# Kernel tuning notes

Hardware: AMD Instinct MI355X
Metric: run time of the kernel (lower is better)

## Reference

```python
import jax, jax.numpy as jnp
import numpy as np

NUM_HEADS = 8
DIM = 256
HEAD_DIM = DIM // NUM_HEADS  # 32
CPB_HIDDEN = 512
FFN_HIDDEN = 1024


def _relative_position_cpb(query_size, key_size, pretrain_size):
    # TransNeXt-style continuous position bias table + index (query==key grid here)
    qh, qw = query_size
    kh, kw = key_size
    ph, pw = pretrain_size
    aqh = np.arange(qh, dtype=np.float64)
    akh = np.arange(kh, dtype=np.float64)
    aqw = np.arange(qw, dtype=np.float64)
    akw = np.arange(kw, dtype=np.float64)
    kH, kW = np.meshgrid(akh, akw, indexing='ij')
    qH, qW = np.meshgrid(aqh, aqw, indexing='ij')
    rel_h = (qH.reshape(-1)[:, None] - kH.reshape(-1)[None, :]) / (ph - 1) * 8.0
    rel_w = (qW.reshape(-1)[:, None] - kW.reshape(-1)[None, :]) / (pw - 1) * 8.0
    rel = np.stack([rel_h, rel_w], axis=-1).reshape(-1, 2)
    table, idx = np.unique(rel, return_inverse=True, axis=0)
    table = np.sign(table) * np.log2(np.abs(table) + 1.0) / np.log2(8.0)
    return idx.astype(np.int32).reshape(-1), table.astype(np.float32)


def setup_inputs() -> dict:
    key = jax.random.key(0)
    ks = jax.random.split(key, 16)
    B, C, H, W = 8, 256, 128, 128
    q = jax.random.normal(ks[0], (B, C, H, W), dtype=jnp.float32)
    kv = jax.random.normal(ks[1], (B, C, H, W), dtype=jnp.float32)
    rel_idx_np, rel_table_np = _relative_position_cpb((32, 32), (32, 32), (32, 32))
    s = 0.02
    inp = {
        'q': q,
        'kv': kv,
        'rel_pos_index': jnp.asarray(rel_idx_np),
        'rel_coords_table': jnp.asarray(rel_table_np),
        'Wq': jax.random.normal(ks[2], (DIM, DIM), jnp.float32) * s,
        'bq': jnp.zeros((DIM,), jnp.float32),
        'Wkv': jax.random.normal(ks[3], (DIM, 2 * DIM), jnp.float32) * s,
        'bkv': jnp.zeros((2 * DIM,), jnp.float32),
        'Wo': jax.random.normal(ks[4], (DIM, DIM), jnp.float32) * s,
        'bo': jnp.zeros((DIM,), jnp.float32),
        'cpb_w1': jax.random.normal(ks[5], (2, CPB_HIDDEN), jnp.float32) * s,
        'cpb_b1': jnp.zeros((CPB_HIDDEN,), jnp.float32),
        'cpb_w2': jax.random.normal(ks[6], (CPB_HIDDEN, NUM_HEADS), jnp.float32) * s,
        'cpb_b2': jnp.zeros((NUM_HEADS,), jnp.float32),
        'ffn_w1': jax.random.normal(ks[7], (DIM, FFN_HIDDEN), jnp.float32) * s,
        'ffn_b1': jnp.zeros((FFN_HIDDEN,), jnp.float32),
        'ffn_w2': jax.random.normal(ks[8], (FFN_HIDDEN, DIM), jnp.float32) * s,
        'ffn_b2': jnp.zeros((DIM,), jnp.float32),
        'ln_g': jnp.ones((DIM,), jnp.float32),
        'ln_b': jnp.zeros((DIM,), jnp.float32),
    }
    return inp


def _resize_bilinear(x, size):
    # matches torch F.interpolate(mode='bilinear', align_corners=False)
    return jax.image.resize(x, (x.shape[0], x.shape[1], size[0], size[1]),
                            method='linear', antialias=False)


def _layernorm(x, g, b, eps=1e-5):
    mu = jnp.mean(x, axis=-1, keepdims=True)
    var = jnp.mean(jnp.square(x - mu), axis=-1, keepdims=True)
    return (x - mu) * jax.lax.rsqrt(var + eps) * g + b


def _fpn_forward(q, kv, rel_pos_index, rel_coords_table, Wq, bq, Wkv, bkv, Wo, bo,
                 cpb_w1, cpb_b1, cpb_w2, cpb_b2, ffn_w1, ffn_b1, ffn_w2, ffn_b2, ln_g, ln_b):
    x = q
    B, C, H, W = q.shape
    pH = H // 4
    pW = H // 4  # note: original code uses h for both, matching square inputs
    N = pH * pW

    qd = jax.nn.relu(_resize_bilinear(q, (pH, pW)))   # [B,C,pH,pW] (dropout p=0)
    kvd = jax.nn.relu(_resize_bilinear(kv, (pH, pW)))
    qt = qd.reshape(B, C, N).transpose(0, 2, 1)   # [B,N,C]
    kvt = kvd.reshape(B, C, N).transpose(0, 2, 1)  # [B,N,C]

    # --- BVAM: cross-attention with continuous relative position bias ---
    qh = (qt @ Wq + bq).reshape(B, N, NUM_HEADS, HEAD_DIM).transpose(0, 2, 1, 3)  # [B,h,N,d]
    kvp = (kvt @ Wkv + bkv).reshape(B, N, 2, NUM_HEADS, HEAD_DIM).transpose(2, 0, 3, 1, 4)
    k, v = kvp[0], kvp[1]  # [B,h,N,d]

    cpb = jax.nn.relu(rel_coords_table @ cpb_w1 + cpb_b1) @ cpb_w2 + cpb_b2  # [L,h]
    bias = cpb[rel_pos_index].reshape(N, N, NUM_HEADS).transpose(2, 0, 1)    # [h,N,N]

    scale = 1.0 / jnp.sqrt(jnp.float32(HEAD_DIM))
    logits = jnp.einsum('bhnd,bhmd->bhnm', qh, k) * scale + bias[None]
    attn = jax.nn.softmax(logits, axis=-1)
    out = jnp.einsum('bhnm,bhmd->bhnd', attn, v)
    out = out.transpose(0, 2, 1, 3).reshape(B, N, C) @ Wo + bo  # [B,N,C]

    # --- FFN (post-norm, gelu) ---
    ff = jax.nn.gelu(out @ ffn_w1 + ffn_b1, approximate=False) @ ffn_w2 + ffn_b2
    y = _layernorm(out + ff, ln_g, ln_b)  # [B,N,C]

    # back to spatial, upsample, residual
    y = y.transpose(0, 2, 1).reshape(B, C, pH, pW)
    y = jax.nn.relu(_resize_bilinear(y, (H, W)))
    return x + y


def reference(q, kv, rel_pos_index, rel_coords_table, Wq, bq, Wkv, bkv, Wo, bo,
              cpb_w1, cpb_b1, cpb_w2, cpb_b2, ffn_w1, ffn_b1, ffn_w2, ffn_b2, ln_g, ln_b):
    return _fpn_forward(q, kv, rel_pos_index, rel_coords_table, Wq, bq, Wkv, bkv, Wo, bo,
                        cpb_w1, cpb_b1, cpb_w2, cpb_b2, ffn_w1, ffn_b1, ffn_w2, ffn_b2, ln_g, ln_b)
```

## Files before the change

kernel.cpp:

```cpp
#include <hip/hip_runtime.h>
#include <hip/hip_bf16.h>
#include <hip/hip_fp16.h>

typedef __hip_bfloat16 bf16;
typedef __attribute__((ext_vector_type(8))) __bf16 bf16x8;
typedef __attribute__((ext_vector_type(4))) __bf16 bf16x4;
typedef __attribute__((ext_vector_type(4))) float f32x4;
typedef __attribute__((ext_vector_type(4))) float f4;

__device__ __forceinline__ void gload_lds16(const bf16* g, bf16* l)
{
    __builtin_amdgcn_global_load_lds((const __attribute__((address_space(1))) void*)g,
                                     (__attribute__((address_space(3))) void*)l, 16, 0, 0);
}

__global__ __launch_bounds__(256) void prep_kernel(
    const float* __restrict__ tab, const float* __restrict__ w1, const float* __restrict__ b1,
    const float* __restrict__ w2, const float* __restrict__ b2, float* __restrict__ cpbout, int L, int ncpb,
    const float* __restrict__ Wq, const float* __restrict__ Wkv, const float* __restrict__ Wo,
    const float* __restrict__ fw1, const float* __restrict__ fw2,
    bf16* __restrict__ WqT, bf16* __restrict__ WkvT, bf16* __restrict__ WoT,
    bf16* __restrict__ W1T, bf16* __restrict__ W2T,
    const float* __restrict__ qsrc, const float* __restrict__ kvsrc,
    bf16* __restrict__ qdst, bf16* __restrict__ kvdst)
{
    __shared__ float o[32][33];
    const int t = threadIdx.x;
    int bid = blockIdx.x;
    if (bid < ncpb) {
        int l = bid * 32 + (t >> 3);
        int js = t & 7;
        bool valid = l < L;
        float t0 = valid ? tab[2 * l] : 0.f, t1 = valid ? tab[2 * l + 1] : 0.f;
        float acc[8];
#pragma unroll
        for (int hh = 0; hh < 8; ++hh) acc[hh] = 0.f;
        for (int j = js; j < 512; j += 8) {
            float hv = fmaxf(t0 * w1[j] + t1 * w1[512 + j] + b1[j], 0.f);
            f4 w2a = *(const f4*)&w2[j * 8];
            f4 w2b = *(const f4*)&w2[j * 8 + 4];
#pragma unroll
            for (int hh = 0; hh < 4; ++hh) { acc[hh] += hv * w2a[hh]; acc[4 + hh] += hv * w2b[hh]; }
        }
#pragma unroll
        for (int d = 1; d < 8; d <<= 1)
#pragma unroll
            for (int hh = 0; hh < 8; ++hh) acc[hh] += __shfl_xor(acc[hh], d);
        if (js == 0 && valid)
#pragma unroll
            for (int hh = 0; hh < 8; ++hh) cpbout[(size_t)hh * L + l] = acc[hh] + b2[hh];
        return;
    }
    bid -= ncpb;
    if (bid < 3072) {
        const float* W; bf16* WT; int K, N, base;
        if (bid < 256)       { W = Wq;  WT = WqT;  K = 256;  N = 256;  base = 0; }
        else if (bid < 768)  { W = Wkv; WT = WkvT; K = 256;  N = 512;  base = 256; }
        else if (bid < 1024) { W = Wo;  WT = WoT;  K = 256;  N = 256;  base = 768; }
        else if (bid < 2048) { W = fw1; WT = W1T;  K = 256;  N = 1024; base = 1024; }
        else                 { W = fw2; WT = W2T;  K = 1024; N = 256;  base = 2048; }
        int idx = (bid - base) * 256 + t;
        int n = idx / K, k = idx % K;
        WT[idx] = (bf16)W[(size_t)k * N + n];
        return;
    }
    bid -= 3072;
    {
        const float* src = bid < 2048 ? qsrc : kvsrc;
        bf16* dst = bid < 2048 ? qdst : kvdst;
        int bb2 = bid & 2047;
        int cc = bb2 & 7, i = (bb2 >> 3) & 31, b = bb2 >> 8;
#pragma unroll
        for (int p = 0; p < 4; ++p) {
            int id = p * 256 + t;
            int c = id >> 5, j = id & 31;
            const float* r = src + ((size_t)(b * 256 + cc * 32 + c) * 128 + 4 * i + 1) * 128 + 4 * j;
            float4 r1 = *(const float4*)r;
            float4 r2 = *(const float4*)(r + 128);
            o[c][j] = 0.25f * (r1.y + r1.z + r2.y + r2.z);
        }
        __syncthreads();
#pragma unroll
        for (int p = 0; p < 4; ++p) {
            int id = p * 256 + t;
            int j = id >> 5, c = id & 31;
            dst[(size_t)(b * 1024 + i * 32 + j) * 256 + cc * 32 + c] = (bf16)fmaxf(o[c][j], 0.f);
        }
    }
}

__global__ __launch_bounds__(256) void bias_gather_kernel(
    const int* __restrict__ ridx, const float* __restrict__ cpbh,
    bf16* __restrict__ biasF, int L)
{
    __shared__ int rix[32][32];
    const int qt = blockIdx.x, mt = blockIdx.y;
    const int t = threadIdx.x;
    {
        int q = t >> 3, m4 = (t & 7) * 4;
        *(int4*)&rix[q][m4] = *(const int4*)&ridx[(size_t)(qt * 32 + q) * 1024 + mt * 32 + m4];
    }
    __syncthreads();
    const int ls = t & 63, qj = (t >> 6) & 1, hg = t >> 7;
    const int lo = ls & 15, hi = ls >> 4;
    int lidx[8];
#pragma unroll
    for (int j = 0; j < 8; ++j) {
        int kf = j >> 2, r = j & 3;
        lidx[j] = rix[qj * 16 + lo][kf * 16 + hi * 4 + r];
    }
#pragma unroll
    for (int hh = 0; hh < 4; ++hh) {
        int h = hg * 4 + hh;
        const float* ct = cpbh + (size_t)h * L;
        bf16 vals[8];
#pragma unroll
        for (int j = 0; j < 8; ++j) vals[j] = (bf16)ct[lidx[j]];
        size_t off = ((((size_t)(h * 32 + qt) * 32 + mt) * 2 + qj) * 64 + ls) * 8;
        *(bf16x8*)&biasF[off] = *(const bf16x8*)vals;
    }
}

template<int BM, int BN>
__device__ __forceinline__ void gemm_core(
    const bf16* __restrict__ A, const bf16* __restrict__ BT, int K,
    int m0, int n0, bf16* As0, bf16* Bs0, f32x4 (&acc)[BM / 32][BN / 32])
{
    constexpr int MI = BM / 32, NJ = BN / 32;
    const int tid = threadIdx.x;
    const int lane = tid & 63, wid = tid >> 6;
    const int lo = lane & 15, hi = lane >> 4;
    const int wr = wid >> 1, wc = wid & 1;
#pragma unroll
    for (int i = 0; i < MI; ++i)
#pragma unroll
        for (int j = 0; j < NJ; ++j) acc[i][j] = f32x4{0.f, 0.f, 0.f, 0.f};

    auto stage = [&](int bsel, int k0) {
        bf16* As = As0 + bsel * (BM * 64);
        bf16* Bs = Bs0 + bsel * (BN * 64);
#pragma unroll
        for (int p = 0; p < BM / 32; ++p) {
            int f = p * 256 + wid * 64 + lane;
            int row = f >> 3, cs = f & 7;
            gload_lds16(&A[(size_t)(m0 + row) * K + k0 + ((cs ^ (row & 7)) * 8)],
                        As + (size_t)(p * 256 + wid * 64) * 8);
        }
#pragma unroll
        for (int p = 0; p < BN / 32; ++p) {
            int f = p * 256 + wid * 64 + lane;
            int row = f >> 3, cs = f & 7;
            gload_lds16(&BT[(size_t)(n0 + row) * K + k0 + ((cs ^ (row & 7)) * 8)],
                        Bs + (size_t)(p * 256 + wid * 64) * 8);
        }
    };
    stage(0, 0);
    __syncthreads();
    const int nt = K / 64;
    int cur = 0;
    for (int t = 0; t < nt; ++t) {
        if (t + 1 < nt) stage(cur ^ 1, (t + 1) * 64);
        const bf16* As = As0 + cur * (BM * 64);
        const bf16* Bs = Bs0 + cur * (BN * 64);
        bf16x8 af[2][MI], bfr[2][NJ];
#pragma unroll
        for (int kk = 0; kk < 2; ++kk) {
#pragma unroll
            for (int i = 0; i < MI; ++i) {
                int row = wr * (BM / 2) + i * 16 + lo;
                af[kk][i] = *(const bf16x8*)&As[row * 64 + (((kk * 4 + hi) ^ (lo & 7)) * 8)];
            }
#pragma unroll
            for (int j = 0; j < NJ; ++j) {
                int row = wc * (BN / 2) + j * 16 + lo;
                bfr[kk][j] = *(const bf16x8*)&Bs[row * 64 + (((kk * 4 + hi) ^ (lo & 7)) * 8)];
            }
        }
#pragma unroll
        for (int kk = 0; kk < 2; ++kk)
#pragma unroll
            for (int i = 0; i < MI; ++i)
#pragma unroll
                for (int j = 0; j < NJ; ++j)
                    acc[i][j] = __builtin_amdgcn_mfma_f32_16x16x32_bf16(af[kk][i], bfr[kk][j], acc[i][j], 0, 0, 0);
        __syncthreads();
        cur ^= 1;
    }
}

template<int BM, int BN>
__global__ __launch_bounds__(256) void gemm_bt(
    const bf16* __restrict__ A, const bf16* __restrict__ BT,
    const float* __restrict__ bias, bf16* __restrict__ Cb, float* __restrict__ Cf,
    const bf16* __restrict__ resid, int M, int N, int K, int act)
{
    constexpr int MI = BM / 32, NJ = BN / 32;
    __shared__ __align__(16) bf16 As[2 * BM * 64];
    __shared__ __align__(16) bf16 Bs[2 * BN * 64];
    const int tid = threadIdx.x;
    const int lane = tid & 63, wid = tid >> 6;
    const int lo = lane & 15, hi = lane >> 4;
    const int m0 = blockIdx.x * BM, n0 = blockIdx.y * BN;
    const int wr = wid >> 1, wc = wid & 1;
    f32x4 acc[MI][NJ];
    gemm_core<BM, BN>(A, BT, K, m0, n0, As, Bs, acc);
#pragma unroll
    for (int i = 0; i < MI; ++i)
#pragma unroll
        for (int j = 0; j < NJ; ++j) {
            int col = n0 + wc * (BN / 2) + j * 16 + lo;
            float bv = bias[col];
#pragma unroll
            for (int r = 0; r < 4; ++r) {
                int row = m0 + wr * (BM / 2) + i * 16 + hi * 4 + r;
                float v = acc[i][j][r] + bv;
                if (act == 1) v = 0.5f * v * (1.f + erff(v * 0.70710678118654752f));
                if (resid) v += (float)resid[(size_t)row * N + col];
                if (Cb) Cb[(size_t)row * N + col] = (bf16)v;
                else    Cf[(size_t)row * N + col] = v;
            }
        }
}

__global__ __launch_bounds__(256) void gemm_qkv(
    const bf16* __restrict__ qt, const bf16* __restrict__ WqT, const float* __restrict__ bq,
    bf16* __restrict__ qhb,
    const bf16* __restrict__ kvt, const bf16* __restrict__ WkvT, const float* __restrict__ bkv,
    bf16* __restrict__ kvpb)
{
    __shared__ __align__(16) bf16 As[2 * 64 * 64];
    __shared__ __align__(16) bf16 Bs[2 * 64 * 64];
    const int tid = threadIdx.x;
    const int lane = tid & 63, wid = tid >> 6;
    const int lo = lane & 15, hi = lane >> 4;
    const int wr = wid >> 1, wc = wid & 1;
    const int by = blockIdx.y;
    const bf16 *A, *BT; const float* bias; bf16* C; int N, n0;
    if (by < 4) { A = qt;  BT = WqT;  bias = bq;  C = qhb;  N = 256; n0 = by * 64; }
    else        { A = kvt; BT = WkvT; bias = bkv; C = kvpb; N = 512; n0 = (by - 4) * 64; }
    const int m0 = blockIdx.x * 64;
    f32x4 acc[2][2];
    gemm_core<64, 64>(A, BT, 256, m0, n0, As, Bs, acc);
#pragma unroll
    for (int i = 0; i < 2; ++i)
#pragma unroll
        for (int j = 0; j < 2; ++j) {
            int col = n0 + wc * 32 + j * 16 + lo;
            float bv = bias[col];
#pragma unroll
            for (int r = 0; r < 4; ++r) {
                int row = m0 + wr * 32 + i * 16 + hi * 4 + r;
                C[(size_t)row * N + col] = (bf16)(acc[i][j][r] + bv);
            }
        }
}

__global__ __launch_bounds__(256) void ffn2_ln_kernel(
    const bf16* __restrict__ A, const bf16* __restrict__ BT,
    const float* __restrict__ bias, const bf16* __restrict__ resid,
    const float* __restrict__ g, const float* __restrict__ bb,
    bf16* __restrict__ ysp)
{
    __shared__ __align__(16) bf16 As[2 * 32 * 64];
    __shared__ __align__(16) bf16 Bs[2 * 256 * 64];
    __shared__ float buf[32][260];
    const int tid = threadIdx.x;
    const int lane = tid & 63, wid = tid >> 6;
    const int lo = lane & 15, hi = lane >> 4;
    const int m0 = blockIdx.x * 32;
    f32x4 acc[2][4];
#pragma unroll
    for (int i = 0; i < 2; ++i)
#pragma unroll
        for (int j = 0; j < 4; ++j) acc[i][j] = f32x4{0.f, 0.f, 0.f, 0.f};

    auto stage = [&](int bsel, int k0) {
        bf16* Asb = As + bsel * (32 * 64);
        bf16* Bsb = Bs + bsel * (256 * 64);
        {
            int f = tid, row = f >> 3, cs = f & 7;
            gload_lds16(&A[(size_t)(m0 + row) * 1024 + k0 + ((cs ^ (row & 7)) * 8)],
                        Asb + (size_t)(wid * 64) * 8);
        }
#pragma unroll
        for (int p = 0; p < 8; ++p) {
            int f = p * 256 + tid, row = f >> 3, cs = f & 7;
            gload_lds16(&BT[(size_t)row * 1024 + k0 + ((cs ^ (row & 7)) * 8)],
                        Bsb + (size_t)(p * 256 + wid * 64) * 8);
        }
    };
    stage(0, 0);
    __syncthreads();
    int cur = 0;
    for (int t = 0; t < 16; ++t) {
        if (t < 15) stage(cur ^ 1, (t + 1) * 64);
        const bf16* Asb = As + cur * (32 * 64);
        const bf16* Bsb = Bs + cur * (256 * 64);
        bf16x8 af[2][2], bfr[2][4];
#pragma unroll
        for (int kk = 0; kk < 2; ++kk) {
#pragma unroll
            for (int i = 0; i < 2; ++i) {
                int row = i * 16 + lo;
                af[kk][i] = *(const bf16x8*)&Asb[row * 64 + (((kk * 4 + hi) ^ (lo & 7)) * 8)];
            }
#pragma unroll
            for (int j = 0; j < 4; ++j) {
                int row = wid * 64 + j * 16 + lo;
                bfr[kk][j] = *(const bf16x8*)&Bsb[row * 64 + (((kk * 4 + hi) ^ (lo & 7)) * 8)];
            }
        }
#pragma unroll
        for (int kk = 0; kk < 2; ++kk)
#pragma unroll
            for (int i = 0; i < 2; ++i)
#pragma unroll
                for (int j = 0; j < 4; ++j)
                    acc[i][j] = __builtin_amdgcn_mfma_f32_16x16x32_bf16(af[kk][i], bfr[kk][j], acc[i][j], 0, 0, 0);
        __syncthreads();
        cur ^= 1;
    }
#pragma unroll
    for (int i = 0; i < 2; ++i)
#pragma unroll
        for (int j = 0; j < 4; ++j) {
            int col = wid * 64 + j * 16 + lo;
            float bv = bias[col];
#pragma unroll
            for (int r = 0; r < 4; ++r) {
                int lr = i * 16 + hi * 4 + r;
                buf[lr][col] = acc[i][j][r] + bv + (float)resid[(size_t)(m0 + lr) * 256 + col];
            }
        }
    __syncthreads();
#pragma unroll
    for (int rr = 0; rr < 8; ++rr) {
        int row = wid * 8 + rr;
        f4 x = *(const f4*)&buf[row][lane * 4];
        float s = x[0] + x[1] + x[2] + x[3];
#pragma unroll
        for (int d = 1; d < 64; d <<= 1) s += __shfl_xor(s, d);
        float mean = s * (1.f / 256.f);
        f4 dv = {x[0] - mean, x[1] - mean, x[2] - mean, x[3] - mean};
        float s2 = dv[0] * dv[0] + dv[1] * dv[1] + dv[2] * dv[2] + dv[3] * dv[3];
#pragma unroll
        for (int d = 1; d < 64; d <<= 1) s2 += __shfl_xor(s2, d);
        float rstd = rsqrtf(s2 * (1.f / 256.f) + 1e-5f);
        f4 o = {dv[0] * rstd, dv[1] * rstd, dv[2] * rstd, dv[3] * rstd};
        *(f4*)&buf[row][lane * 4] = o;
    }
    __syncthreads();
    float gc = g[tid], bc = bb[tid];
    int b = m0 >> 10, n0l = m0 & 1023;
    bf16* dst = &ysp[((size_t)(b * 256 + tid) << 10) + n0l];
#pragma unroll
    for (int p = 0; p < 4; ++p) {
        bf16 tmp[8];
#pragma unroll
        for (int k = 0; k < 8; ++k) tmp[k] = (bf16)(buf[p * 8 + k][tid] * gc + bc);
        *(bf16x8*)&dst[p * 8] = *(const bf16x8*)tmp;
    }
}

__global__ __launch_bounds__(256) void vtrans_kernel(const bf16* __restrict__ kvp,
                                                     bf16* __restrict__ vT)
{
    __shared__ __align__(16) bf16 tile[64][40];
    int bid = blockIdx.x;
    int mc = bid & 15, h = (bid >> 4) & 7, b = bid >> 7;
    int t = threadIdx.x;
    {
        int m = t >> 2, p = (t & 3) * 8;
        *(float4*)&tile[m][p] =
            *(const float4*)&kvp[(size_t)(b * 1024 + mc * 64 + m) * 512 + 256 + h * 32 + p];
    }
    __syncthreads();
#pragma unroll
    for (int it = 0; it < 8; ++it) {
        int f = it * 256 + t;
        int d = f >> 6, m = f & 63;
        vT[(size_t)((b * 8 + h) * 32 + d) * 1024 + mc * 64 + m] = tile[m][d];
    }
}

__global__ __launch_bounds__(256) void attn_kernel(
    const bf16* __restrict__ qh, const bf16* __restrict__ kvp, const bf16* __restrict__ vT,
    const bf16* __restrict__ biasF, bf16* __restrict__ attnout)
{
    __shared__ __align__(16) bf16 Ps[4][32 * 40];
    __shared__ __align__(16) __half accs[4][32][34];
    __shared__ float pm[4][32], pl[4][32];
    const int tid = threadIdx.x, lane = tid & 63, wid = tid >> 6;
    const int lo = lane & 15, hi = lane >> 4;
    const int qt = blockIdx.x, n0 = qt * 32;
    const int h = blockIdx.y;
    const int b = blockIdx.z;
    const float scale = 0.17677669529663687f;
    const f32x4 zero4 = {0.f, 0.f, 0.f, 0.f};

    bf16x8 qf[2];
#pragma unroll
    for (int qj = 0; qj < 2; ++qj)
        qf[qj] = *(const bf16x8*)&qh[(size_t)(b * 1024 + n0 + qj * 16 + lo) * 256 + h * 32 + hi * 8];

    f32x4 acc[2][2];
#pragma unroll
    for (int i = 0; i < 2; ++i)
#pragma unroll
        for (int j = 0; j < 2; ++j) acc[i][j] = zero4;
    float mrow[2] = {-1e30f, -1e30f}, lrow[2] = {0.f, 0.f};

    bf16* Pw = Ps[wid];

    for (int t = wid; t < 32; t += 4) {
        const int m0 = t * 32;
        bf16x8 kfr0 = *(const bf16x8*)&kvp[(size_t)(b * 1024 + m0 + lo) * 512 + h * 32 + hi * 8];
        bf16x8 kfr1 = *(const bf16x8*)&kvp[(size_t)(b * 1024 + m0 + 16 + lo) * 512 + h * 32 + hi * 8];
        bf16x8 va0 = *(const bf16x8*)&vT[(size_t)((b * 8 + h) * 32 + lo) * 1024 + m0 + hi * 8];
        bf16x8 va1 = *(const bf16x8*)&vT[(size_t)((b * 8 + h) * 32 + 16 + lo) * 1024 + m0 + hi * 8];
        size_t boff = (((size_t)(h * 32 + qt) * 32 + t) * 2 * 64 + lane) * 8;
        bf16x8 bv0 = *(const bf16x8*)&biasF[boff];
        bf16x8 bv1 = *(const bf16x8*)&biasF[boff + 512];

        f32x4 s[2][2];
        s[0][0] = __builtin_amdgcn_mfma_f32_16x16x32_bf16(kfr0, qf[0], zero4, 0, 0, 0);
        s[0][1] = __builtin_amdgcn_mfma_f32_16x16x32_bf16(kfr0, qf[1], zero4, 0, 0, 0);
        s[1][0] = __builtin_amdgcn_mfma_f32_16x16x32_bf16(kfr1, qf[0], zero4, 0, 0, 0);
        s[1][1] = __builtin_amdgcn_mfma_f32_16x16x32_bf16(kfr1, qf[1], zero4, 0, 0, 0);
#pragma unroll
        for (int kf = 0; kf < 2; ++kf)
#pragma unroll
            for (int r = 0; r < 4; ++r) {
                s[kf][0][r] = s[kf][0][r] * scale + (float)bv0[kf * 4 + r];
                s[kf][1][r] = s[kf][1][r] * scale + (float)bv1[kf * 4 + r];
            }
#pragma unroll
        for (int qj = 0; qj < 2; ++qj) {
            float mx = fmaxf(fmaxf(fmaxf(s[0][qj][0], s[0][qj][1]), fmaxf(s[0][qj][2], s[0][qj][3])),
                             fmaxf(fmaxf(s[1][qj][0], s[1][qj][1]), fmaxf(s[1][qj][2], s[1][qj][3])));
            mx = fmaxf(mx, __shfl_xor(mx, 16));
            mx = fmaxf(mx, __shfl_xor(mx, 32));
            float mnew = fmaxf(mrow[qj], mx);
            float alpha = __expf(mrow[qj] - mnew);
            float rs = 0.f;
#pragma unroll
            for (int kf = 0; kf < 2; ++kf)
#pragma unroll
                for (int r = 0; r < 4; ++r) {
                    float p = __expf(s[kf][qj][r] - mnew);
                    s[kf][qj][r] = p;
                    rs += p;
                }
            rs += __shfl_xor(rs, 16);
            rs += __shfl_xor(rs, 32);
            lrow[qj] = lrow[qj] * alpha + rs;
            mrow[qj] = mnew;
#pragma unroll
            for (int di = 0; di < 2; ++di)
#pragma unroll
                for (int r = 0; r < 4; ++r) acc[di][qj][r] *= alpha;
        }
#pragma unroll
        for (int qj = 0; qj < 2; ++qj)
#pragma unroll
            for (int kf = 0; kf < 2; ++kf)
#pragma unroll
                for (int r = 0; r < 4; ++r)
                    Pw[(qj * 16 + lo) * 40 + kf * 16 + hi * 4 + r] = (bf16)s[kf][qj][r];
        bf16x8 pb0 = *(const bf16x8*)&Pw[lo * 40 + hi * 8];
        bf16x8 pb1 = *(const bf16x8*)&Pw[(16 + lo) * 40 + hi * 8];
        acc[0][0] = __builtin_amdgcn_mfma_f32_16x16x32_bf16(va0, pb0, acc[0][0], 0, 0, 0);
        acc[0][1] = __builtin_amdgcn_mfma_f32_16x16x32_bf16(va0, pb1, acc[0][1], 0, 0, 0);
        acc[1][0] = __builtin_amdgcn_mfma_f32_16x16x32_bf16(va1, pb0, acc[1][0], 0, 0, 0);
        acc[1][1] = __builtin_amdgcn_mfma_f32_16x16x32_bf16(va1, pb1, acc[1][1], 0, 0, 0);
    }
#pragma unroll
    for (int di = 0; di < 2; ++di)
#pragma unroll
        for (int qj = 0; qj < 2; ++qj)
#pragma unroll
            for (int r = 0; r < 4; ++r)
                accs[wid][di * 16 + hi * 4 + r][qj * 16 + lo] = __float2half(acc[di][qj][r]);
    if (hi == 0) {
#pragma unroll
        for (int qj = 0; qj < 2; ++qj) {
            pm[wid][qj * 16 + lo] = mrow[qj];
            pl[wid][qj * 16 + lo] = lrow[qj];
        }
    }
    __syncthreads();
    int q = tid >> 3, d0 = (tid & 7) * 4;
    float M = fmaxf(fmaxf(pm[0][q], pm[1][q]), fmaxf(pm[2][q], pm[3][q]));
    float f0 = __expf(pm[0][q] - M), f1 = __expf(pm[1][q] - M);
    float f2 = __expf(pm[2][q] - M), f3 = __expf(pm[3][q] - M);
    float inv = 1.f / (pl[0][q] * f0 + pl[1][q] * f1 + pl[2][q] * f2 + pl[3][q] * f3);
    bf16 tmp[4];
#pragma unroll
    for (int j = 0; j < 4; ++j) {
        int d = d0 + j;
        float o = f0 * (float)accs[0][d][q] + f1 * (float)accs[1][d][q] +
                  f2 * (float)accs[2][d][q] + f3 * (float)accs[3][d][q];
        tmp[j] = (bf16)(o * inv);
    }
    *(bf16x4*)&attnout[(size_t)(b * 1024 + n0 + q) * 256 + h * 32 + d0] = *(const bf16x4*)tmp;
}

__global__ __launch_bounds__(256) void upsample_kernel(const float* __restrict__ x,
    const bf16* __restrict__ ysp, float* __restrict__ out)
{
    int idx = blockIdx.x * 256 + threadIdx.x;
    int w4 = idx & 31; int r1 = idx >> 5;
    int hh = r1 & 127; int r2 = r1 >> 7;
    int c = r2 & 255; int b = r2 >> 8;
    float chh = 0.25f * hh - 0.375f;
    float fi = floorf(chh);
    float fh = chh - fi;
    int i0 = (int)fi;
    int ia = i0 < 0 ? 0 : i0;
    int ib = (i0 + 1) > 31 ? 31 : (i0 + 1);
    const bf16* yr = ysp + ((size_t)(b * 256 + c) << 10);
    const bf16* ra = yr + ia * 32;
    const bf16* rb = yr + ib * 32;
    f4 xv = *(const f4*)&x[(size_t)idx * 4];
    f4 o;
#pragma unroll
    for (int k = 0; k < 4; ++k) {
        int ww = w4 * 4 + k;
        float cww = 0.25f * ww - 0.375f;
        float fj = floorf(cww);
        float fw = cww - fj;
        int j0 = (int)fj;
        int ja = j0 < 0 ? 0 : j0;
        int jb = (j0 + 1) > 31 ? 31 : (j0 + 1);
        float v = (1.f - fh) * ((1.f - fw) * (float)ra[ja] + fw * (float)ra[jb]) +
                  fh * ((1.f - fw) * (float)rb[ja] + fw * (float)rb[jb]);
        o[k] = xv[k] + fmaxf(v, 0.f);
    }
    *(f4*)&out[(size_t)idx * 4] = o;
}

extern "C" void kernel_launch(void* const* d_in, const int* in_sizes, int n_in,
                              void* d_out, int out_size, void* d_ws, size_t ws_size,
                              hipStream_t stream)
{
    (void)n_in; (void)out_size; (void)ws_size;
    const float* q    = (const float*)d_in[0];
    const float* kv   = (const float*)d_in[1];
    const int*   ridx = (const int*)d_in[2];
    const float* rtab = (const float*)d_in[3];
    const float* Wq   = (const float*)d_in[4];
    const float* bq   = (const float*)d_in[5];
    const float* Wkv  = (const float*)d_in[6];
    const float* bkv  = (const float*)d_in[7];
    const float* Wo   = (const float*)d_in[8];
    const float* bo   = (const float*)d_in[9];
    const float* cw1  = (const float*)d_in[10];
    const float* cb1  = (const float*)d_in[11];
    const float* cw2  = (const float*)d_in[12];
    const float* cb2  = (const float*)d_in[13];
    const float* fw1  = (const float*)d_in[14];
    const float* fb1  = (const float*)d_in[15];
    const float* fw2  = (const float*)d_in[16];
    const float* fb2  = (const float*)d_in[17];
    const float* lng  = (const float*)d_in[18];
    const float* lnb  = (const float*)d_in[19];
    const int L = in_sizes[3] / 2;
    const int ncpb = (L + 31) / 32;

    char* w = (char*)d_ws;
    auto alloc = [&](size_t bytes) { char* p = w; w += (bytes + 255) & ~(size_t)255; return p; };
    bf16* qt      = (bf16*)alloc(8192ull * 256 * 2);
    bf16* kvt     = (bf16*)alloc(8192ull * 256 * 2);
    bf16* qhb     = (bf16*)alloc(8192ull * 256 * 2);
    bf16* kvpb    = (bf16*)alloc(8192ull * 512 * 2);
    bf16* vTb     = (bf16*)alloc(8ull * 8 * 32 * 1024 * 2);
    bf16* attnb   = (bf16*)alloc(8192ull * 256 * 2);
    bf16* outb    = (bf16*)alloc(8192ull * 256 * 2);
    bf16* ffh     = (bf16*)alloc(8192ull * 1024 * 2);
    bf16* ysp     = (bf16*)alloc(8ull * 256 * 1024 * 2);
    bf16* WqT     = (bf16*)alloc(256ull * 256 * 2);
    bf16* WkvT    = (bf16*)alloc(512ull * 256 * 2);
    bf16* WoT     = (bf16*)alloc(256ull * 256 * 2);
    bf16* W1T     = (bf16*)alloc(1024ull * 256 * 2);
    bf16* W2T     = (bf16*)alloc(256ull * 1024 * 2);
    float* cpbb   = (float*)alloc((size_t)8 * L * 4);
    bf16* biasF   = ffh;

    prep_kernel<<<dim3(ncpb + 3072 + 4096), 256, 0, stream>>>(
        rtab, cw1, cb1, cw2, cb2, cpbb, L, ncpb,
        Wq, Wkv, Wo, fw1, fw2, WqT, WkvT, WoT, W1T, W2T,
        q, kv, qt, kvt);
    bias_gather_kernel<<<dim3(32, 32), 256, 0, stream>>>(ridx, cpbb, biasF, L);
    gemm_qkv<<<dim3(128, 12), 256, 0, stream>>>(qt, WqT, bq, qhb, kvt, WkvT, bkv, kvpb);
    vtrans_kernel<<<dim3(1024), 256, 0, stream>>>(kvpb, vTb);
    attn_kernel<<<dim3(32, 8, 8), 256, 0, stream>>>(qhb, kvpb, vTb, biasF, attnb);
    gemm_bt<64, 64><<<dim3(128, 4), 256, 0, stream>>>(attnb, WoT, bo, outb, nullptr, nullptr, 8192, 256, 256, 0);
    gemm_bt<128, 64><<<dim3(64, 16), 256, 0, stream>>>(outb, W1T, fb1, ffh, nullptr, nullptr, 8192, 1024, 256, 1);
    ffn2_ln_kernel<<<dim3(256), 256, 0, stream>>>(ffh, W2T, fb2, outb, lng, lnb, ysp);
    upsample_kernel<<<dim3(32768), 256, 0, stream>>>(q, ysp, (float*)d_out);
}
```

Measured before the change: 202.2 us.

## Fuse V transpose into QKV GEMM epilogue and single-buffer GEMM LDS

```diff
diff --git a/kernel.cpp b/kernel.cpp
--- a/kernel.cpp
+++ b/kernel.cpp
@@ -124,7 +124,7 @@
 template<int BM, int BN>
 __device__ __forceinline__ void gemm_core(
     const bf16* __restrict__ A, const bf16* __restrict__ BT, int K,
-    int m0, int n0, bf16* As0, bf16* Bs0, f32x4 (&acc)[BM / 32][BN / 32])
+    int m0, int n0, bf16* As, bf16* Bs, f32x4 (&acc)[BM / 32][BN / 32])
 {
     constexpr int MI = BM / 32, NJ = BN / 32;
     const int tid = threadIdx.x;
@@ -136,9 +136,8 @@
 #pragma unroll
         for (int j = 0; j < NJ; ++j) acc[i][j] = f32x4{0.f, 0.f, 0.f, 0.f};
 
-    auto stage = [&](int bsel, int k0) {
-        bf16* As = As0 + bsel * (BM * 64);
-        bf16* Bs = Bs0 + bsel * (BN * 64);
+    for (int k0 = 0; k0 < K; k0 += 64) {
+        __syncthreads();
 #pragma unroll
         for (int p = 0; p < BM / 32; ++p) {
             int f = p * 256 + wid * 64 + lane;
@@ -153,15 +152,7 @@
             gload_lds16(&BT[(size_t)(n0 + row) * K + k0 + ((cs ^ (row & 7)) * 8)],
                         Bs + (size_t)(p * 256 + wid * 64) * 8);
         }
-    };
-    stage(0, 0);
-    __syncthreads();
-    const int nt = K / 64;
-    int cur = 0;
-    for (int t = 0; t < nt; ++t) {
-        if (t + 1 < nt) stage(cur ^ 1, (t + 1) * 64);
-        const bf16* As = As0 + cur * (BM * 64);
-        const bf16* Bs = Bs0 + cur * (BN * 64);
+        __syncthreads();
         bf16x8 af[2][MI], bfr[2][NJ];
 #pragma unroll
         for (int kk = 0; kk < 2; ++kk) {
@@ -183,8 +174,6 @@
 #pragma unroll
                 for (int j = 0; j < NJ; ++j)
                     acc[i][j] = __builtin_amdgcn_mfma_f32_16x16x32_bf16(af[kk][i], bfr[kk][j], acc[i][j], 0, 0, 0);
-        __syncthreads();
-        cur ^= 1;
     }
 }
 
@@ -195,8 +184,8 @@
     const bf16* __restrict__ resid, int M, int N, int K, int act)
 {
     constexpr int MI = BM / 32, NJ = BN / 32;
-    __shared__ __align__(16) bf16 As[2 * BM * 64];
-    __shared__ __align__(16) bf16 Bs[2 * BN * 64];
+    __shared__ __align__(16) bf16 As[BM * 64];
+    __shared__ __align__(16) bf16 Bs[BN * 64];
     const int tid = threadIdx.x;
     const int lane = tid & 63, wid = tid >> 6;
     const int lo = lane & 15, hi = lane >> 4;
@@ -226,18 +215,18 @@
     const bf16* __restrict__ qt, const bf16* __restrict__ WqT, const float* __restrict__ bq,
     bf16* __restrict__ qhb,
     const bf16* __restrict__ kvt, const bf16* __restrict__ WkvT, const float* __restrict__ bkv,
-    bf16* __restrict__ kvpb)
-{
-    __shared__ __align__(16) bf16 As[2 * 64 * 64];
-    __shared__ __align__(16) bf16 Bs[2 * 64 * 64];
+    bf16* __restrict__ kvpb, bf16* __restrict__ vT)
+{
+    __shared__ __align__(16) bf16 As[64 * 64];
+    __shared__ __align__(16) bf16 Bs[64 * 64];
     const int tid = threadIdx.x;
     const int lane = tid & 63, wid = tid >> 6;
     const int lo = lane & 15, hi = lane >> 4;
     const int wr = wid >> 1, wc = wid & 1;
     const int by = blockIdx.y;
-    const bf16 *A, *BT; const float* bias; bf16* C; int N, n0;
-    if (by < 4) { A = qt;  BT = WqT;  bias = bq;  C = qhb;  N = 256; n0 = by * 64; }
-    else        { A = kvt; BT = WkvT; bias = bkv; C = kvpb; N = 512; n0 = (by - 4) * 64; }
+    const bf16 *A, *BT; const float* bias; int n0;
+    if (by < 4)      { A = qt;  BT = WqT;  bias = bq;  n0 = by * 64; }
+    else             { A = kvt; BT = WkvT; bias = bkv; n0 = (by - 4) * 64; }
     const int m0 = blockIdx.x * 64;
     f32x4 acc[2][2];
     gemm_core<64, 64>(A, BT, 256, m0, n0, As, Bs, acc);
@@ -247,10 +236,27 @@
         for (int j = 0; j < 2; ++j) {
             int col = n0 + wc * 32 + j * 16 + lo;
             float bv = bias[col];
-#pragma unroll
-            for (int r = 0; r < 4; ++r) {
-                int row = m0 + wr * 32 + i * 16 + hi * 4 + r;
-                C[(size_t)row * N + col] = (bf16)(acc[i][j][r] + bv);
+            if (by < 4) {
+#pragma unroll
+                for (int r = 0; r < 4; ++r) {
+                    int row = m0 + wr * 32 + i * 16 + hi * 4 + r;
+                    qhb[(size_t)row * 256 + col] = (bf16)(acc[i][j][r] + bv);
+                }
+            } else if (by < 8) {
+#pragma unroll
+                for (int r = 0; r < 4; ++r) {
+                    int row = m0 + wr * 32 + i * 16 + hi * 4 + r;
+                    kvpb[(size_t)row * 512 + col] = (bf16)(acc[i][j][r] + bv);
+                }
+            } else {
+                int vcol = col - 256;
+                int h = vcol >> 5, d = vcol & 31;
+                int b = m0 >> 10;
+                int mbase = (m0 & 1023) + wr * 32 + i * 16 + hi * 4;
+                bf16 tmp[4];
+#pragma unroll
+                for (int r = 0; r < 4; ++r) tmp[r] = (bf16)(acc[i][j][r] + bv);
+                *(bf16x4*)&vT[(size_t)((b * 8 + h) * 32 + d) * 1024 + mbase] = *(const bf16x4*)tmp;
             }
         }
 }
@@ -261,8 +267,8 @@
     const float* __restrict__ g, const float* __restrict__ bb,
     bf16* __restrict__ ysp)
 {
-    __shared__ __align__(16) bf16 As[2 * 32 * 64];
-    __shared__ __align__(16) bf16 Bs[2 * 256 * 64];
+    __shared__ __align__(16) bf16 As[32 * 64];
+    __shared__ __align__(16) bf16 Bs[256 * 64];
     __shared__ float buf[32][260];
     const int tid = threadIdx.x;
     const int lane = tid & 63, wid = tid >> 6;
@@ -274,40 +280,32 @@
 #pragma unroll
         for (int j = 0; j < 4; ++j) acc[i][j] = f32x4{0.f, 0.f, 0.f, 0.f};
 
-    auto stage = [&](int bsel, int k0) {
-        bf16* Asb = As + bsel * (32 * 64);
-        bf16* Bsb = Bs + bsel * (256 * 64);
+    for (int k0 = 0; k0 < 1024; k0 += 64) {
+        __syncthreads();
         {
             int f = tid, row = f >> 3, cs = f & 7;
             gload_lds16(&A[(size_t)(m0 + row) * 1024 + k0 + ((cs ^ (row & 7)) * 8)],
-                        Asb + (size_t)(wid * 64) * 8);
+                        As + (size_t)(wid * 64) * 8);
         }
 #pragma unroll
         for (int p = 0; p < 8; ++p) {
             int f = p * 256 + tid, row = f >> 3, cs = f & 7;
             gload_lds16(&BT[(size_t)row * 1024 + k0 + ((cs ^ (row & 7)) * 8)],
-                        Bsb + (size_t)(p * 256 + wid * 64) * 8);
-        }
-    };
-    stage(0, 0);
-    __syncthreads();
-    int cur = 0;
-    for (int t = 0; t < 16; ++t) {
-        if (t < 15) stage(cur ^ 1, (t + 1) * 64);
-        const bf16* Asb = As + cur * (32 * 64);
-        const bf16* Bsb = Bs + cur * (256 * 64);
+                        Bs + (size_t)(p * 256 + wid * 64) * 8);
+        }
+        __syncthreads();
         bf16x8 af[2][2], bfr[2][4];
 #pragma unroll
         for (int kk = 0; kk < 2; ++kk) {
 #pragma unroll
             for (int i = 0; i < 2; ++i) {
                 int row = i * 16 + lo;
-                af[kk][i] = *(const bf16x8*)&Asb[row * 64 + (((kk * 4 + hi) ^ (lo & 7)) * 8)];
+                af[kk][i] = *(const bf16x8*)&As[row * 64 + (((kk * 4 + hi) ^ (lo & 7)) * 8)];
             }
 #pragma unroll
             for (int j = 0; j < 4; ++j) {
                 int row = wid * 64 + j * 16 + lo;
-                bfr[kk][j] = *(const bf16x8*)&Bsb[row * 64 + (((kk * 4 + hi) ^ (lo & 7)) * 8)];
+                bfr[kk][j] = *(const bf16x8*)&Bs[row * 64 + (((kk * 4 + hi) ^ (lo & 7)) * 8)];
             }
         }
 #pragma unroll
@@ -317,8 +315,6 @@
 #pragma unroll
                 for (int j = 0; j < 4; ++j)
                     acc[i][j] = __builtin_amdgcn_mfma_f32_16x16x32_bf16(af[kk][i], bfr[kk][j], acc[i][j], 0, 0, 0);
-        __syncthreads();
-        cur ^= 1;
     }
 #pragma unroll
     for (int i = 0; i < 2; ++i)
@@ -359,27 +355,6 @@
 #pragma unroll
         for (int k = 0; k < 8; ++k) tmp[k] = (bf16)(buf[p * 8 + k][tid] * gc + bc);
         *(bf16x8*)&dst[p * 8] = *(const bf16x8*)tmp;
-    }
-}
-
-__global__ __launch_bounds__(256) void vtrans_kernel(const bf16* __restrict__ kvp,
-                                                     bf16* __restrict__ vT)
-{
-    __shared__ __align__(16) bf16 tile[64][40];
-    int bid = blockIdx.x;
-    int mc = bid & 15, h = (bid >> 4) & 7, b = bid >> 7;
-    int t = threadIdx.x;
-    {
-        int m = t >> 2, p = (t & 3) * 8;
-        *(float4*)&tile[m][p] =
-            *(const float4*)&kvp[(size_t)(b * 1024 + mc * 64 + m) * 512 + 256 + h * 32 + p];
-    }
-    __syncthreads();
-#pragma unroll
-    for (int it = 0; it < 8; ++it) {
-        int f = it * 256 + t;
-        int d = f >> 6, m = f & 63;
-        vT[(size_t)((b * 8 + h) * 32 + d) * 1024 + mc * 64 + m] = tile[m][d];
     }
 }
 
@@ -591,8 +566,7 @@
         Wq, Wkv, Wo, fw1, fw2, WqT, WkvT, WoT, W1T, W2T,
         q, kv, qt, kvt);
     bias_gather_kernel<<<dim3(32, 32), 256, 0, stream>>>(ridx, cpbb, biasF, L);
-    gemm_qkv<<<dim3(128, 12), 256, 0, stream>>>(qt, WqT, bq, qhb, kvt, WkvT, bkv, kvpb);
-    vtrans_kernel<<<dim3(1024), 256, 0, stream>>>(kvpb, vTb);
+    gemm_qkv<<<dim3(128, 12), 256, 0, stream>>>(qt, WqT, bq, qhb, kvt, WkvT, bkv, kvpb, vTb);
     attn_kernel<<<dim3(32, 8, 8), 256, 0, stream>>>(qhb, kvpb, vTb, biasF, attnb);
     gemm_bt<64, 64><<<dim3(128, 4), 256, 0, stream>>>(attnb, WoT, bo, outb, nullptr, nullptr, 8192, 256, 256, 0);
     gemm_bt<128, 64><<<dim3(64, 16), 256, 0, stream>>>(outb, W1T, fb1, ffh, nullptr, nullptr, 8192, 1024, 256, 1);
```

Measured after the change: 190.5 us. 5.8% less time.
